# Performance work log

Hardware: AMD Instinct MI355X
Metric: run time of the kernel (lower is better)

## Reference

```python
import jax, jax.numpy as jnp
import numpy as np

N = 50000
ALPHA = 0.1
LAMDA = 0.5


def setup_inputs() -> dict:
    key = jax.random.key(0)
    ks = jax.random.split(key, 8)
    E, IN, H, C, L = 800000, 512, 128, 40, 8
    features = jax.random.normal(ks[0], (N, IN), dtype=jnp.float32)
    edge_index = jax.random.randint(ks[1], (2, E), 0, N, dtype=jnp.int32)
    norm_A = jax.random.uniform(ks[2], (E,), dtype=jnp.float32) * 0.1
    w_fc0 = jax.random.normal(ks[3], (IN, H), dtype=jnp.float32) / np.sqrt(IN)
    b_fc0 = jnp.zeros((H,), dtype=jnp.float32)
    conv_w = jax.random.normal(ks[4], (L, H, H), dtype=jnp.float32) / np.sqrt(H)
    w_fc1 = jax.random.normal(ks[5], (H, C), dtype=jnp.float32) / np.sqrt(H)
    b_fc1 = jnp.zeros((C,), dtype=jnp.float32)
    return {"features": features, "edge_index": edge_index, "norm_A": norm_A,
            "w_fc0": w_fc0, "b_fc0": b_fc0, "conv_w": conv_w,
            "w_fc1": w_fc1, "b_fc1": b_fc1}


def _spmm(edge_index, w, x):
    # y[dst] += w_e * x[src]  over all edges; x: [N, H]
    src, dst = edge_index[0], edge_index[1]
    msgs = x[src] * w[:, None]                      # [E, H]
    return jax.ops.segment_sum(msgs, dst, num_segments=N)


def reference(features, edge_index, norm_A, w_fc0, b_fc0, conv_w, w_fc1, b_fc1):
    # dropout p=0.0 -> identity
    x = jax.nn.relu(features @ w_fc0 + b_fc0)       # [N, H]
    h0 = x
    L = conv_w.shape[0]
    for i in range(L):
        l = i + 1
        beta = jnp.log(LAMDA / l + 1.0).astype(x.dtype)
        hi = _spmm(edge_index, norm_A, x)           # Â x
        support = (1.0 - ALPHA) * hi + ALPHA * h0   # initial residual
        # identity mapping: beta * (support W) + (1-beta) * support
        x = jax.nn.relu(beta * (support @ conv_w[i]) + (1.0 - beta) * support)
    return x @ w_fc1 + b_fc1                        # [N, C]
```

## Files before the change

kernel.cpp:

```cpp
#include <hip/hip_runtime.h>
#include <hip/hip_bf16.h>
#include <math.h>

#define N_NODES 50000
#define M_PAD   50048
#define E_EDGES 800000
#define IN_DIM  512
#define HDIM    128
#define CDIM    40
#define LAYERS  8
#define NB      196

typedef __attribute__((ext_vector_type(8))) short short8;
typedef __attribute__((ext_vector_type(4))) float floatx4;
typedef unsigned short ushort_t;

__device__ inline float bf2f(unsigned short u) {
    return __uint_as_float(((unsigned)u) << 16);
}
__device__ inline unsigned short f2bf(float v) {
    __hip_bfloat16 b = __float2bfloat16(v);
    return *reinterpret_cast<unsigned short*>(&b);
}


__global__ void hist_kernel(const int* __restrict__ dst, int* __restrict__ cnt) {
    int i = blockIdx.x * blockDim.x + threadIdx.x;
    if (i < E_EDGES) atomicAdd(&cnt[dst[i]], 1);
}

__global__ void scanA(const int* __restrict__ cnt, int* __restrict__ bsum) {
    __shared__ int sm[256];
    int t = threadIdx.x, i = blockIdx.x * 256 + t;
    sm[t] = (i < N_NODES) ? cnt[i] : 0;
    __syncthreads();
    for (int d = 128; d > 0; d >>= 1) {
        if (t < d) sm[t] += sm[t + d];
        __syncthreads();
    }
    if (t == 0) bsum[blockIdx.x] = sm[0];
}

__global__ void scanB(const int* __restrict__ bsum, int* __restrict__ boff) {
    __shared__ int sm[256];
    int t = threadIdx.x;
    sm[t] = (t < NB) ? bsum[t] : 0;
    __syncthreads();
    for (int d = 1; d < 256; d <<= 1) {
        int v = (t >= d) ? sm[t - d] : 0;
        __syncthreads();
        sm[t] += v;
        __syncthreads();
    }
    if (t < NB) boff[t] = (t > 0) ? sm[t - 1] : 0;
}

__global__ void scanC(const int* __restrict__ cnt, const int* __restrict__ boff,
                      int* __restrict__ row_start, int* __restrict__ cursor) {
    __shared__ int sm[256];
    int t = threadIdx.x, i = blockIdx.x * 256 + t;
    int v = (i < N_NODES) ? cnt[i] : 0;
    sm[t] = v;
    __syncthreads();
    for (int d = 1; d < 256; d <<= 1) {
        int x = (t >= d) ? sm[t - d] : 0;
        __syncthreads();
        sm[t] += x;
        __syncthreads();
    }
    if (i < N_NODES) {
        int incl = boff[blockIdx.x] + sm[t];
        int excl = incl - v;
        row_start[i] = excl;
        cursor[i]    = excl;
        if (i == N_NODES - 1) row_start[N_NODES] = incl;
    }
}

__global__ void scatter_kernel(const int* __restrict__ ei, const float* __restrict__ normA,
                               int* __restrict__ cursor, int2* __restrict__ perm) {
    int i = blockIdx.x * blockDim.x + threadIdx.x;
    if (i >= E_EDGES) return;
    int d = ei[E_EDGES + i];
    int idx = atomicAdd(&cursor[d], 1);
    perm[idx] = make_int2(ei[i], __float_as_int(normA[i]));
}


__global__ void prep_weights(const float* __restrict__ W0, const float* __restrict__ convW,
                             const float* __restrict__ W1,
                             ushort_t* __restrict__ Wt0, ushort_t* __restrict__ WtL,
                             ushort_t* __restrict__ Wt1) {
    int i = blockIdx.x * blockDim.x + threadIdx.x;
    if (i < 128 * 512) {
        int n = i >> 9, k = i & 511;
        Wt0[i] = f2bf(W0[k * HDIM + n]);
        return;
    }
    int j = i - 128 * 512;
    if (j < 8 * 128 * 128) {
        int l = j >> 14, rem = j & 16383, n = rem >> 7, k = rem & 127;
        WtL[j] = f2bf(convW[l * 16384 + k * HDIM + n]);
        return;
    }
    int m = j - 8 * 128 * 128;
    if (m < 48 * 128) {
        int n = m >> 7, k = m & 127;
        Wt1[m] = (n < CDIM) ? f2bf(W1[k * CDIM + n]) : (ushort_t)0;
    }
}


__global__ __launch_bounds__(256)
void fc0_mfma(const float* __restrict__ F, const ushort_t* __restrict__ Wt0,
              const float* __restrict__ b0, ushort_t* __restrict__ h0b) {
    __shared__ float sA[2][32 * 128];
    int t = threadIdx.x;
    int wave = t >> 6, lane = t & 63;
    int quad = lane >> 4, l16 = lane & 15;
    int R0 = blockIdx.x * 32;

    const ushort_t* bbase = Wt0 + (size_t)(wave * 32 + l16) * IN_DIM + quad * 8;

    floatx4 acc[2][2];
#pragma unroll
    for (int rf = 0; rf < 2; rf++)
#pragma unroll
        for (int nt = 0; nt < 2; nt++) acc[rf][nt] = (floatx4){0.f, 0.f, 0.f, 0.f};

    auto stage = [&](int cc, int buf) {
#pragma unroll
        for (int i = 0; i < 4; i++) {
            int X = i * 4096 + wave * 1024 + lane * 16;
            int row = X >> 9;
            int colb = (X & 511) ^ ((row & 7) << 4);
            int gr = R0 + row; if (gr > N_NODES - 1) gr = N_NODES - 1;
            const float* src = F + (size_t)gr * IN_DIM + cc * 128 + (colb >> 2);
            __builtin_amdgcn_global_load_lds(
                (const __attribute__((address_space(1))) unsigned int*)src,
                (__attribute__((address_space(3))) unsigned int*)&sA[buf][i * 1024 + wave * 256],
                16, 0, 0);
        }
    };

    stage(0, 0);

    int mask = (l16 & 7) << 4;
    int ib0 = ((quad << 5) ^ mask) >> 2;
    int ib1 = (((quad << 5) | 16) ^ mask) >> 2;

#pragma unroll
    for (int cc = 0; cc < 4; cc++) {
        __syncthreads();
        if (cc < 3) stage(cc + 1, (cc + 1) & 1);
        const float* bufp = &sA[cc & 1][0];
        const float* r0p = bufp + l16 * 128;
        const float* r1p = bufp + (l16 + 16) * 128;
#pragma unroll
        for (int k2 = 0; k2 < 4; k2++) {
            int ks = cc * 4 + k2;
            float4 f00 = *(const float4*)(r0p + k2 * 32 + ib0);
            float4 f01 = *(const float4*)(r0p + k2 * 32 + ib1);
            float4 f10 = *(const float4*)(r1p + k2 * 32 + ib0);
            float4 f11 = *(const float4*)(r1p + k2 * 32 + ib1);
            short8 a0, a1;
            a0[0] = (short)f2bf(f00.x); a0[1] = (short)f2bf(f00.y);
            a0[2] = (short)f2bf(f00.z); a0[3] = (short)f2bf(f00.w);
            a0[4] = (short)f2bf(f01.x); a0[5] = (short)f2bf(f01.y);
            a0[6] = (short)f2bf(f01.z); a0[7] = (short)f2bf(f01.w);
            a1[0] = (short)f2bf(f10.x); a1[1] = (short)f2bf(f10.y);
            a1[2] = (short)f2bf(f10.z); a1[3] = (short)f2bf(f10.w);
            a1[4] = (short)f2bf(f11.x); a1[5] = (short)f2bf(f11.y);
            a1[6] = (short)f2bf(f11.z); a1[7] = (short)f2bf(f11.w);
#pragma unroll
            for (int nt = 0; nt < 2; nt++) {
                short8 b = *(const short8*)(bbase + (size_t)nt * 16 * IN_DIM + ks * 32);
                acc[0][nt] = __builtin_amdgcn_mfma_f32_16x16x32_bf16(a0, b, acc[0][nt], 0, 0, 0);
                acc[1][nt] = __builtin_amdgcn_mfma_f32_16x16x32_bf16(a1, b, acc[1][nt], 0, 0, 0);
            }
        }
    }

#pragma unroll
    for (int nt = 0; nt < 2; nt++) {
        int col = wave * 32 + nt * 16 + l16;
        float bias = b0[col];
#pragma unroll
        for (int r = 0; r < 4; r++) {
            int row = R0 + quad * 4 + r;
            float v = acc[0][nt][r] + bias;
            v = v > 0.f ? v : 0.f;
            h0b[(size_t)row * HDIM + col] = f2bf(v);
        }
#pragma unroll
        for (int r = 0; r < 4; r++) {
            int row = R0 + 16 + quad * 4 + r;
            float v = acc[1][nt][r] + bias;
            v = v > 0.f ? v : 0.f;
            h0b[(size_t)row * HDIM + col] = f2bf(v);
        }
    }
}


#define SROW 136

__device__ __forceinline__ void spmm_proc32(int2 pa, int2 pb,
                                            const ushort_t* __restrict__ xb,
                                            int sl, float* __restrict__ acc) {
#pragma unroll
    for (int j = 0; j < 16; j += 4) {
        int   a0 = __shfl(pa.x, j + 0, 16), b0 = __shfl(pb.x, j + 0, 16);
        int   a1 = __shfl(pa.x, j + 1, 16), b1 = __shfl(pb.x, j + 1, 16);
        int   a2 = __shfl(pa.x, j + 2, 16), b2 = __shfl(pb.x, j + 2, 16);
        int   a3 = __shfl(pa.x, j + 3, 16), b3 = __shfl(pb.x, j + 3, 16);
        float wa0 = __int_as_float(__shfl(pa.y, j + 0, 16));
        float wa1 = __int_as_float(__shfl(pa.y, j + 1, 16));
        float wa2 = __int_as_float(__shfl(pa.y, j + 2, 16));
        float wa3 = __int_as_float(__shfl(pa.y, j + 3, 16));
        float wb0 = __int_as_float(__shfl(pb.y, j + 0, 16));
        float wb1 = __int_as_float(__shfl(pb.y, j + 1, 16));
        float wb2 = __int_as_float(__shfl(pb.y, j + 2, 16));
        float wb3 = __int_as_float(__shfl(pb.y, j + 3, 16));
        short8 va0 = *(const short8*)(xb + (size_t)a0 * HDIM + sl * 8);
        short8 vb0 = *(const short8*)(xb + (size_t)b0 * HDIM + sl * 8);
        short8 va1 = *(const short8*)(xb + (size_t)a1 * HDIM + sl * 8);
        short8 vb1 = *(const short8*)(xb + (size_t)b1 * HDIM + sl * 8);
        short8 va2 = *(const short8*)(xb + (size_t)a2 * HDIM + sl * 8);
        short8 vb2 = *(const short8*)(xb + (size_t)b2 * HDIM + sl * 8);
        short8 va3 = *(const short8*)(xb + (size_t)a3 * HDIM + sl * 8);
        short8 vb3 = *(const short8*)(xb + (size_t)b3 * HDIM + sl * 8);
#pragma unroll
        for (int c = 0; c < 8; c++) {
            acc[c] += wa0 * bf2f((ushort_t)va0[c]);
            acc[c] += wa1 * bf2f((ushort_t)va1[c]);
            acc[c] += wa2 * bf2f((ushort_t)va2[c]);
            acc[c] += wa3 * bf2f((ushort_t)va3[c]);
            acc[c] += wb0 * bf2f((ushort_t)vb0[c]);
            acc[c] += wb1 * bf2f((ushort_t)vb1[c]);
            acc[c] += wb2 * bf2f((ushort_t)vb2[c]);
            acc[c] += wb3 * bf2f((ushort_t)vb3[c]);
        }
    }
}

__global__ __launch_bounds__(256)
void layer_fused(const int* __restrict__ row_start, const int2* __restrict__ perm,
                 const ushort_t* __restrict__ xb, const ushort_t* __restrict__ h0b,
                 const ushort_t* __restrict__ Wt, ushort_t* __restrict__ X,
                 float beta) {
    __shared__ short sS[64][SROW];
    int t = threadIdx.x;
    int wave = t >> 6, lane = t & 63;
    int grp = lane >> 4, sl = lane & 15;
    int quad = lane >> 4, l16 = lane & 15;
    int row0 = blockIdx.x * 64;
    int G = wave * 4 + grp;
    int Rg = row0 + G * 4;

    int rbv = 0;
    if (sl <= 4) {
        int idx = Rg + sl; if (idx > N_NODES) idx = N_NODES;
        rbv = row_start[idx];
    }
    int e0[4], e1[4];
#pragma unroll
    for (int r = 0; r < 4; r++) {
        e0[r] = __shfl(rbv, r, 16);
        e1[r] = __shfl(rbv, r + 1, 16);
    }

    int2 pA = make_int2(0, 0), pB = make_int2(0, 0);
    if (e0[0] + sl < e1[0])      pA = perm[e0[0] + sl];
    if (e0[0] + 16 + sl < e1[0]) pB = perm[e0[0] + 16 + sl];

#pragma unroll
    for (int r = 0; r < 4; r++) {
        int row = Rg + r;

        short8 h;
#pragma unroll
        for (int c = 0; c < 8; c++) h[c] = 0;
        if (row < N_NODES) h = *(const short8*)(h0b + (size_t)row * HDIM + sl * 8);

        int2 nA = make_int2(0, 0), nB = make_int2(0, 0);
        if (r < 3) {
            if (e0[r + 1] + sl < e1[r + 1])      nA = perm[e0[r + 1] + sl];
            if (e0[r + 1] + 16 + sl < e1[r + 1]) nB = perm[e0[r + 1] + 16 + sl];
        }

        float acc[8];
#pragma unroll
        for (int c = 0; c < 8; c++) acc[c] = 0.f;

        spmm_proc32(pA, pB, xb, sl, acc);

        for (int chunk = e0[r] + 32; chunk < e1[r]; chunk += 32) {
            int2 qa = make_int2(0, 0), qb = make_int2(0, 0);
            if (chunk + sl < e1[r])      qa = perm[chunk + sl];
            if (chunk + 16 + sl < e1[r]) qb = perm[chunk + 16 + sl];
            spmm_proc32(qa, qb, xb, sl, acc);
        }

        short8 o;
        if (row < N_NODES) {
#pragma unroll
            for (int c = 0; c < 8; c++)
                o[c] = (short)f2bf(0.9f * acc[c] + 0.1f * bf2f((ushort_t)h[c]));
        } else {
#pragma unroll
            for (int c = 0; c < 8; c++) o[c] = 0;
        }
        *(short8*)&sS[G * 4 + r][sl * 8] = o;

        pA = nA; pB = nB;
    }

    short8 afrag[4];
#pragma unroll
    for (int ks = 0; ks < 4; ks++)
        afrag[ks] = *(const short8*)&sS[wave * 16 + l16][ks * 32 + quad * 8];

    floatx4 gacc[8];
#pragma unroll
    for (int nt = 0; nt < 8; nt++) {
        const ushort_t* bp = Wt + (size_t)(nt * 16 + l16) * HDIM + quad * 8;
        floatx4 c = (floatx4){0.f, 0.f, 0.f, 0.f};
#pragma unroll
        for (int ks = 0; ks < 4; ks++) {
            short8 b = *(const short8*)(bp + ks * 32);
            c = __builtin_amdgcn_mfma_f32_16x16x32_bf16(afrag[ks], b, c, 0, 0, 0);
        }
        gacc[nt] = c;
    }
    float g = 1.f - beta;
#pragma unroll
    for (int nt = 0; nt < 8; nt++) {
        int col = nt * 16 + l16;
#pragma unroll
        for (int r = 0; r < 4; r++) {
            int lrow = wave * 16 + quad * 4 + r;
            float s = bf2f((ushort_t)sS[lrow][col]);
            float v = beta * gacc[nt][r] + g * s;
            v = v > 0.f ? v : 0.f;
            X[(size_t)(row0 + lrow) * HDIM + col] = f2bf(v);
        }
    }
}


__global__ void fc1_mfma(const ushort_t* __restrict__ X, const ushort_t* __restrict__ Wt1,
                         const float* __restrict__ b1, float* __restrict__ out) {
    int wave = threadIdx.x >> 6;
    int lane = threadIdx.x & 63;
    int quad = lane >> 4, l16 = lane & 15;
    int row0 = blockIdx.x * 64 + wave * 16;

    int arow = row0 + l16; if (arow > N_NODES - 1) arow = N_NODES - 1;
    const ushort_t* ap = X + (size_t)arow * HDIM + quad * 8;
    short8 afrag[4];
#pragma unroll
    for (int ks = 0; ks < 4; ks++) afrag[ks] = *(const short8*)(ap + ks * 32);

    floatx4 acc[3];
#pragma unroll
    for (int nt = 0; nt < 3; nt++) {
        const ushort_t* bp = Wt1 + (size_t)(nt * 16 + l16) * HDIM + quad * 8;
        floatx4 c = (floatx4){0.f, 0.f, 0.f, 0.f};
#pragma unroll
        for (int ks = 0; ks < 4; ks++) {
            short8 b = *(const short8*)(bp + ks * 32);
            c = __builtin_amdgcn_mfma_f32_16x16x32_bf16(afrag[ks], b, c, 0, 0, 0);
        }
        acc[nt] = c;
    }
#pragma unroll
    for (int nt = 0; nt < 3; nt++) {
        int col = nt * 16 + l16;
        if (col < CDIM) {
            float bias = b1[col];
#pragma unroll
            for (int r = 0; r < 4; r++) {
                int row = row0 + quad * 4 + r;
                if (row < N_NODES)
                    out[(size_t)row * CDIM + col] = acc[nt][r] + bias;
            }
        }
    }
}


extern "C" void kernel_launch(void* const* d_in, const int* in_sizes, int n_in,
                              void* d_out, int out_size, void* d_ws, size_t ws_size,
                              hipStream_t stream) {
    const float* F     = (const float*)d_in[0];
    const int*   ei    = (const int*)d_in[1];
    const float* normA = (const float*)d_in[2];
    const float* W0    = (const float*)d_in[3];
    const float* b0    = (const float*)d_in[4];
    const float* convW = (const float*)d_in[5];
    const float* W1    = (const float*)d_in[6];
    const float* b1    = (const float*)d_in[7];
    float*       out   = (float*)d_out;

    ushort_t* h0b  = (ushort_t*)d_ws;
    ushort_t* xab  = h0b + (size_t)M_PAD * HDIM;
    ushort_t* xbb  = xab + (size_t)M_PAD * HDIM;
    ushort_t* Wt0  = xbb + (size_t)M_PAD * HDIM;
    ushort_t* WtL  = Wt0 + 128 * 512;
    ushort_t* Wt1  = WtL + 8 * 128 * 128;
    int*   row_start = (int*)(Wt1 + 48 * 128);
    int*   cursor    = row_start + (N_NODES + 8);
    int*   cnt       = cursor + (N_NODES + 8);
    int*   bsum      = cnt + (N_NODES + 8);
    int*   boff      = bsum + 256;
    int2*  perm      = (int2*)(boff + 256);

    hipMemsetAsync(cnt, 0, N_NODES * sizeof(int), stream);
    hist_kernel<<<(E_EDGES + 255) / 256, 256, 0, stream>>>(ei + E_EDGES, cnt);
    scanA<<<NB, 256, 0, stream>>>(cnt, bsum);
    scanB<<<1, 256, 0, stream>>>(bsum, boff);
    scanC<<<NB, 256, 0, stream>>>(cnt, boff, row_start, cursor);
    scatter_kernel<<<(E_EDGES + 255) / 256, 256, 0, stream>>>(ei, normA, cursor, perm);
    prep_weights<<<(128 * 512 + 8 * 128 * 128 + 48 * 128 + 255) / 256, 256, 0, stream>>>(
        W0, convW, W1, Wt0, WtL, Wt1);

    fc0_mfma<<<M_PAD / 32, 256, 0, stream>>>(F, Wt0, b0, h0b);

    ushort_t* ping = h0b;
    ushort_t* pong = xab;
    for (int i = 0; i < LAYERS; i++) {
        float beta = logf(0.5f / (float)(i + 1) + 1.0f);
        layer_fused<<<M_PAD / 64, 256, 0, stream>>>(
            row_start, perm, ping, h0b, WtL + (size_t)i * HDIM * HDIM, pong, beta);
        if (i == 0) { ping = xab; pong = xbb; }
        else { ushort_t* tmp = ping; ping = pong; pong = tmp; }
    }
    fc1_mfma<<<M_PAD / 64, 256, 0, stream>>>(ping, Wt1, b1, out);
}
```

Before: 651.1 us.

## Triple-buffer fc0 LDS staging and bound first SpMM chunk by degree

The fc0 GEMM moves from double to triple buffering of the feature tiles. It waits with a partial vmcnt plus a raw barrier instead of a full __syncthreads, so two stages of global-to-LDS loads stay in flight. In the SpMM layer kernel, the first 32-edge chunk is processed only up to the row's actual degree, in groups of 8 neighbours with shuffled indices and weights. This avoids gathering padding entries for low-degree rows. The trade-offs are more LDS per block and a hand-tuned waitcnt count that must match the number of loads each stage issues.

```diff
diff --git a/kernel.cpp b/kernel.cpp
--- a/kernel.cpp
+++ b/kernel.cpp
@@ -114,7 +114,7 @@
 __global__ __launch_bounds__(256)
 void fc0_mfma(const float* __restrict__ F, const ushort_t* __restrict__ Wt0,
               const float* __restrict__ b0, ushort_t* __restrict__ h0b) {
-    __shared__ float sA[2][32 * 128];
+    __shared__ float sA[3][32 * 128];
     int t = threadIdx.x;
     int wave = t >> 6, lane = t & 63;
     int quad = lane >> 4, l16 = lane & 15;
@@ -144,6 +144,7 @@
     };
 
     stage(0, 0);
+    stage(1, 1);
 
     int mask = (l16 & 7) << 4;
     int ib0 = ((quad << 5) ^ mask) >> 2;
@@ -151,9 +152,11 @@
 
 #pragma unroll
     for (int cc = 0; cc < 4; cc++) {
-        __syncthreads();
-        if (cc < 3) stage(cc + 1, (cc + 1) & 1);
-        const float* bufp = &sA[cc & 1][0];
+        asm volatile("s_waitcnt vmcnt(4)" ::: "memory");
+        __builtin_amdgcn_s_barrier();
+        __builtin_amdgcn_sched_barrier(0);
+        if (cc < 2) stage(cc + 2, (cc + 2) % 3);
+        const float* bufp = &sA[cc % 3][0];
         const float* r0p = bufp + l16 * 128;
         const float* r1p = bufp + (l16 + 16) * 128;
 #pragma unroll
@@ -293,7 +296,44 @@
 #pragma unroll
         for (int c = 0; c < 8; c++) acc[c] = 0.f;
 
-        spmm_proc32(pA, pB, xb, sl, acc);
+        int deg = e1[r] - e0[r];
+        int n = deg < 32 ? deg : 32;
+        for (int j = 0; j < n; j += 8) {
+            int2 pL = (j < 16) ? pA : pB;
+            int2 pH = (j + 4 < 16) ? pA : pB;
+            int jl = j & 15, jh = (j + 4) & 15;
+            int   a0 = __shfl(pL.x, jl + 0, 16), b0 = __shfl(pH.x, jh + 0, 16);
+            int   a1 = __shfl(pL.x, jl + 1, 16), b1 = __shfl(pH.x, jh + 1, 16);
+            int   a2 = __shfl(pL.x, jl + 2, 16), b2 = __shfl(pH.x, jh + 2, 16);
+            int   a3 = __shfl(pL.x, jl + 3, 16), b3 = __shfl(pH.x, jh + 3, 16);
+            float wa0 = __int_as_float(__shfl(pL.y, jl + 0, 16));
+            float wa1 = __int_as_float(__shfl(pL.y, jl + 1, 16));
+            float wa2 = __int_as_float(__shfl(pL.y, jl + 2, 16));
+            float wa3 = __int_as_float(__shfl(pL.y, jl + 3, 16));
+            float wb0 = __int_as_float(__shfl(pH.y, jh + 0, 16));
+            float wb1 = __int_as_float(__shfl(pH.y, jh + 1, 16));
+            float wb2 = __int_as_float(__shfl(pH.y, jh + 2, 16));
+            float wb3 = __int_as_float(__shfl(pH.y, jh + 3, 16));
+            short8 va0 = *(const short8*)(xb + (size_t)a0 * HDIM + sl * 8);
+            short8 vb0 = *(const short8*)(xb + (size_t)b0 * HDIM + sl * 8);
+            short8 va1 = *(const short8*)(xb + (size_t)a1 * HDIM + sl * 8);
+            short8 vb1 = *(const short8*)(xb + (size_t)b1 * HDIM + sl * 8);
+            short8 va2 = *(const short8*)(xb + (size_t)a2 * HDIM + sl * 8);
+            short8 vb2 = *(const short8*)(xb + (size_t)b2 * HDIM + sl * 8);
+            short8 va3 = *(const short8*)(xb + (size_t)a3 * HDIM + sl * 8);
+            short8 vb3 = *(const short8*)(xb + (size_t)b3 * HDIM + sl * 8);
+#pragma unroll
+            for (int c = 0; c < 8; c++) {
+                acc[c] += wa0 * bf2f((ushort_t)va0[c]);
+                acc[c] += wa1 * bf2f((ushort_t)va1[c]);
+                acc[c] += wa2 * bf2f((ushort_t)va2[c]);
+                acc[c] += wa3 * bf2f((ushort_t)va3[c]);
+                acc[c] += wb0 * bf2f((ushort_t)vb0[c]);
+                acc[c] += wb1 * bf2f((ushort_t)vb1[c]);
+                acc[c] += wb2 * bf2f((ushort_t)vb2[c]);
+                acc[c] += wb3 * bf2f((ushort_t)vb3[c]);
+            }
+        }
 
         for (int chunk = e0[r] + 32; chunk < e1[r]; chunk += 32) {
             int2 qa = make_int2(0, 0), qb = make_int2(0, 0);
```

Measured after the change: 645.6 us. No clear change (-0.8%).

## Triple-buffer fc0 staging and process SpMM rows in pairs for more loads in flight

Applied to the files above, without the earlier changes.

The fc0 GEMM moves from a double-buffered LDS pipeline to a triple-buffered one. It issues two stages ahead and uses explicit vmcnt waits plus raw barriers instead of __syncthreads. The fused layer kernel now aggregates two destination rows at once through a new spmm_pair helper, so 16 gathers are in flight per step instead of 8, which is meant to hide gather latency. The cost is more registers and LDS, which may lower occupancy, and rows with more than 32 edges still fall back to sequential per-row loops.

```diff
diff --git a/kernel.cpp b/kernel.cpp
--- a/kernel.cpp
+++ b/kernel.cpp
@@ -114,7 +114,7 @@
 __global__ __launch_bounds__(256)
 void fc0_mfma(const float* __restrict__ F, const ushort_t* __restrict__ Wt0,
               const float* __restrict__ b0, ushort_t* __restrict__ h0b) {
-    __shared__ float sA[2][32 * 128];
+    __shared__ float sA[3][32 * 128];
     int t = threadIdx.x;
     int wave = t >> 6, lane = t & 63;
     int quad = lane >> 4, l16 = lane & 15;
@@ -144,6 +144,7 @@
     };
 
     stage(0, 0);
+    stage(1, 1);
 
     int mask = (l16 & 7) << 4;
     int ib0 = ((quad << 5) ^ mask) >> 2;
@@ -151,9 +152,11 @@
 
 #pragma unroll
     for (int cc = 0; cc < 4; cc++) {
-        __syncthreads();
-        if (cc < 3) stage(cc + 1, (cc + 1) & 1);
-        const float* bufp = &sA[cc & 1][0];
+        asm volatile("s_waitcnt vmcnt(4)" ::: "memory");
+        __builtin_amdgcn_s_barrier();
+        __builtin_amdgcn_sched_barrier(0);
+        if (cc < 2) stage(cc + 2, (cc + 2) % 3);
+        const float* bufp = &sA[cc % 3][0];
         const float* r0p = bufp + l16 * 128;
         const float* r1p = bufp + (l16 + 16) * 128;
 #pragma unroll
@@ -244,6 +247,74 @@
     }
 }
 
+__device__ __forceinline__ void spmm_pair(int2 pa0, int2 pb0, int2 pa1, int2 pb1,
+                                          const ushort_t* __restrict__ xb, int sl,
+                                          float* __restrict__ accA,
+                                          float* __restrict__ accB) {
+#pragma unroll
+    for (int j = 0; j < 16; j += 4) {
+        int   xa0 = __shfl(pa0.x, j + 0, 16), ya0 = __shfl(pb0.x, j + 0, 16);
+        int   xa1 = __shfl(pa0.x, j + 1, 16), ya1 = __shfl(pb0.x, j + 1, 16);
+        int   xa2 = __shfl(pa0.x, j + 2, 16), ya2 = __shfl(pb0.x, j + 2, 16);
+        int   xa3 = __shfl(pa0.x, j + 3, 16), ya3 = __shfl(pb0.x, j + 3, 16);
+        int   xb0i = __shfl(pa1.x, j + 0, 16), yb0 = __shfl(pb1.x, j + 0, 16);
+        int   xb1i = __shfl(pa1.x, j + 1, 16), yb1 = __shfl(pb1.x, j + 1, 16);
+        int   xb2i = __shfl(pa1.x, j + 2, 16), yb2 = __shfl(pb1.x, j + 2, 16);
+        int   xb3i = __shfl(pa1.x, j + 3, 16), yb3 = __shfl(pb1.x, j + 3, 16);
+        short8 u0 = *(const short8*)(xb + (size_t)xa0 * HDIM + sl * 8);
+        short8 u1 = *(const short8*)(xb + (size_t)xa1 * HDIM + sl * 8);
+        short8 u2 = *(const short8*)(xb + (size_t)xa2 * HDIM + sl * 8);
+        short8 u3 = *(const short8*)(xb + (size_t)xa3 * HDIM + sl * 8);
+        short8 u4 = *(const short8*)(xb + (size_t)ya0 * HDIM + sl * 8);
+        short8 u5 = *(const short8*)(xb + (size_t)ya1 * HDIM + sl * 8);
+        short8 u6 = *(const short8*)(xb + (size_t)ya2 * HDIM + sl * 8);
+        short8 u7 = *(const short8*)(xb + (size_t)ya3 * HDIM + sl * 8);
+        short8 w0 = *(const short8*)(xb + (size_t)xb0i * HDIM + sl * 8);
+        short8 w1 = *(const short8*)(xb + (size_t)xb1i * HDIM + sl * 8);
+        short8 w2 = *(const short8*)(xb + (size_t)xb2i * HDIM + sl * 8);
+        short8 w3 = *(const short8*)(xb + (size_t)xb3i * HDIM + sl * 8);
+        short8 w4 = *(const short8*)(xb + (size_t)yb0 * HDIM + sl * 8);
+        short8 w5 = *(const short8*)(xb + (size_t)yb1 * HDIM + sl * 8);
+        short8 w6 = *(const short8*)(xb + (size_t)yb2 * HDIM + sl * 8);
+        short8 w7 = *(const short8*)(xb + (size_t)yb3 * HDIM + sl * 8);
+        float fa0 = __int_as_float(__shfl(pa0.y, j + 0, 16));
+        float fa1 = __int_as_float(__shfl(pa0.y, j + 1, 16));
+        float fa2 = __int_as_float(__shfl(pa0.y, j + 2, 16));
+        float fa3 = __int_as_float(__shfl(pa0.y, j + 3, 16));
+        float fa4 = __int_as_float(__shfl(pb0.y, j + 0, 16));
+        float fa5 = __int_as_float(__shfl(pb0.y, j + 1, 16));
+        float fa6 = __int_as_float(__shfl(pb0.y, j + 2, 16));
+        float fa7 = __int_as_float(__shfl(pb0.y, j + 3, 16));
+        float fb0 = __int_as_float(__shfl(pa1.y, j + 0, 16));
+        float fb1 = __int_as_float(__shfl(pa1.y, j + 1, 16));
+        float fb2 = __int_as_float(__shfl(pa1.y, j + 2, 16));
+        float fb3 = __int_as_float(__shfl(pa1.y, j + 3, 16));
+        float fb4 = __int_as_float(__shfl(pb1.y, j + 0, 16));
+        float fb5 = __int_as_float(__shfl(pb1.y, j + 1, 16));
+        float fb6 = __int_as_float(__shfl(pb1.y, j + 2, 16));
+        float fb7 = __int_as_float(__shfl(pb1.y, j + 3, 16));
+#pragma unroll
+        for (int c = 0; c < 8; c++) {
+            accA[c] += fa0 * bf2f((ushort_t)u0[c]);
+            accA[c] += fa1 * bf2f((ushort_t)u1[c]);
+            accA[c] += fa2 * bf2f((ushort_t)u2[c]);
+            accA[c] += fa3 * bf2f((ushort_t)u3[c]);
+            accA[c] += fa4 * bf2f((ushort_t)u4[c]);
+            accA[c] += fa5 * bf2f((ushort_t)u5[c]);
+            accA[c] += fa6 * bf2f((ushort_t)u6[c]);
+            accA[c] += fa7 * bf2f((ushort_t)u7[c]);
+            accB[c] += fb0 * bf2f((ushort_t)w0[c]);
+            accB[c] += fb1 * bf2f((ushort_t)w1[c]);
+            accB[c] += fb2 * bf2f((ushort_t)w2[c]);
+            accB[c] += fb3 * bf2f((ushort_t)w3[c]);
+            accB[c] += fb4 * bf2f((ushort_t)w4[c]);
+            accB[c] += fb5 * bf2f((ushort_t)w5[c]);
+            accB[c] += fb6 * bf2f((ushort_t)w6[c]);
+            accB[c] += fb7 * bf2f((ushort_t)w7[c]);
+        }
+    }
+}
+
 __global__ __launch_bounds__(256)
 void layer_fused(const int* __restrict__ row_start, const int2* __restrict__ perm,
                  const ushort_t* __restrict__ xb, const ushort_t* __restrict__ h0b,
@@ -270,50 +341,73 @@
         e1[r] = __shfl(rbv, r + 1, 16);
     }
 
-    int2 pA = make_int2(0, 0), pB = make_int2(0, 0);
-    if (e0[0] + sl < e1[0])      pA = perm[e0[0] + sl];
-    if (e0[0] + 16 + sl < e1[0]) pB = perm[e0[0] + 16 + sl];
-
-#pragma unroll
-    for (int r = 0; r < 4; r++) {
-        int row = Rg + r;
-
-        short8 h;
-#pragma unroll
-        for (int c = 0; c < 8; c++) h[c] = 0;
-        if (row < N_NODES) h = *(const short8*)(h0b + (size_t)row * HDIM + sl * 8);
-
-        int2 nA = make_int2(0, 0), nB = make_int2(0, 0);
-        if (r < 3) {
-            if (e0[r + 1] + sl < e1[r + 1])      nA = perm[e0[r + 1] + sl];
-            if (e0[r + 1] + 16 + sl < e1[r + 1]) nB = perm[e0[r + 1] + 16 + sl];
-        }
-
-        float acc[8];
-#pragma unroll
-        for (int c = 0; c < 8; c++) acc[c] = 0.f;
-
-        spmm_proc32(pA, pB, xb, sl, acc);
-
-        for (int chunk = e0[r] + 32; chunk < e1[r]; chunk += 32) {
+    int2 cA0 = make_int2(0, 0), cB0 = make_int2(0, 0);
+    int2 cA1 = make_int2(0, 0), cB1 = make_int2(0, 0);
+    if (e0[0] + sl < e1[0])      cA0 = perm[e0[0] + sl];
+    if (e0[0] + 16 + sl < e1[0]) cB0 = perm[e0[0] + 16 + sl];
+    if (e0[1] + sl < e1[1])      cA1 = perm[e0[1] + sl];
+    if (e0[1] + 16 + sl < e1[1]) cB1 = perm[e0[1] + 16 + sl];
+
+#pragma unroll
+    for (int p = 0; p < 2; p++) {
+        int ra = 2 * p, rb = 2 * p + 1;
+        int rowa = Rg + ra, rowb = Rg + rb;
+
+        short8 ha, hb;
+#pragma unroll
+        for (int c = 0; c < 8; c++) { ha[c] = 0; hb[c] = 0; }
+        if (rowa < N_NODES) ha = *(const short8*)(h0b + (size_t)rowa * HDIM + sl * 8);
+        if (rowb < N_NODES) hb = *(const short8*)(h0b + (size_t)rowb * HDIM + sl * 8);
+
+        int2 nA0 = make_int2(0, 0), nB0 = make_int2(0, 0);
+        int2 nA1 = make_int2(0, 0), nB1 = make_int2(0, 0);
+        if (p == 0) {
+            if (e0[2] + sl < e1[2])      nA0 = perm[e0[2] + sl];
+            if (e0[2] + 16 + sl < e1[2]) nB0 = perm[e0[2] + 16 + sl];
+            if (e0[3] + sl < e1[3])      nA1 = perm[e0[3] + sl];
+            if (e0[3] + 16 + sl < e1[3]) nB1 = perm[e0[3] + 16 + sl];
+        }
+
+        float accA[8], accB[8];
+#pragma unroll
+        for (int c = 0; c < 8; c++) { accA[c] = 0.f; accB[c] = 0.f; }
+
+        spmm_pair(cA0, cB0, cA1, cB1, xb, sl, accA, accB);
+
+        for (int chunk = e0[ra] + 32; chunk < e1[ra]; chunk += 32) {
             int2 qa = make_int2(0, 0), qb = make_int2(0, 0);
-            if (chunk + sl < e1[r])      qa = perm[chunk + sl];
-            if (chunk + 16 + sl < e1[r]) qb = perm[chunk + 16 + sl];
-            spmm_proc32(qa, qb, xb, sl, acc);
-        }
-
-        short8 o;
-        if (row < N_NODES) {
+            if (chunk + sl < e1[ra])      qa = perm[chunk + sl];
+            if (chunk + 16 + sl < e1[ra]) qb = perm[chunk + 16 + sl];
+            spmm_proc32(qa, qb, xb, sl, accA);
+        }
+        for (int chunk = e0[rb] + 32; chunk < e1[rb]; chunk += 32) {
+            int2 qa = make_int2(0, 0), qb = make_int2(0, 0);
+            if (chunk + sl < e1[rb])      qa = perm[chunk + sl];
+            if (chunk + 16 + sl < e1[rb]) qb = perm[chunk + 16 + sl];
+            spmm_proc32(qa, qb, xb, sl, accB);
+        }
+
+        short8 oa, ob;
+        if (rowa < N_NODES) {
 #pragma unroll
             for (int c = 0; c < 8; c++)
-                o[c] = (short)f2bf(0.9f * acc[c] + 0.1f * bf2f((ushort_t)h[c]));
+                oa[c] = (short)f2bf(0.9f * accA[c] + 0.1f * bf2f((ushort_t)ha[c]));
         } else {
 #pragma unroll
-            for (int c = 0; c < 8; c++) o[c] = 0;
-        }
-        *(short8*)&sS[G * 4 + r][sl * 8] = o;
-
-        pA = nA; pB = nB;
+            for (int c = 0; c < 8; c++) oa[c] = 0;
+        }
+        if (rowb < N_NODES) {
+#pragma unroll
+            for (int c = 0; c < 8; c++)
+                ob[c] = (short)f2bf(0.9f * accB[c] + 0.1f * bf2f((ushort_t)hb[c]));
+        } else {
+#pragma unroll
+            for (int c = 0; c < 8; c++) ob[c] = 0;
+        }
+        *(short8*)&sS[G * 4 + ra][sl * 8] = oa;
+        *(short8*)&sS[G * 4 + rb][sl * 8] = ob;
+
+        cA0 = nA0; cB0 = nB0; cA1 = nA1; cB1 = nB1;
     }
 
     short8 afrag[4];
```

New measurement: 748.4 us. 1.15x slower.
